# Optimization experiments

Measured on AMD Instinct MI355X. Metric: run time of the kernel, lower is better.

The kernel has to match this reference:

```python
import jax, jax.numpy as jnp
from jax import lax
import numpy as np
import itertools

R = 7            # resolution
N = R * R        # 49 tokens
H = 8            # num_heads
KD = 32          # key_dim
QKD = 2 * H * KD # 512
VD = 2 * KD * H  # 512 (attn_ratio * key_dim * num_heads)
DIM = 384
B = 2048
SCALE = KD ** (-0.5)
BN_EPS = 1e-5


def _bias_idxs():
    points = list(itertools.product(range(R), range(R)))
    offsets = {}
    idxs = []
    for p1 in points:
        for p2 in points:
            o = (abs(p1[0] - p2[0]), abs(p1[1] - p2[1]))
            if o not in offsets:
                offsets[o] = len(offsets)
            idxs.append(offsets[o])
    return np.asarray(idxs, dtype=np.int32).reshape(N, N)  # [49,49], values in [0,49)


def setup_inputs() -> dict:
    key = jax.random.key(0)
    ks = jax.random.split(key, 8)
    return {
        "x": jax.random.normal(ks[0], (B, N, DIM), jnp.float32),
        "pwconv_w": jax.random.normal(ks[1], (QKD + VD, DIM), jnp.float32) * 0.05,
        "pwconv_b": jax.random.normal(ks[2], (QKD + VD,), jnp.float32) * 0.05,
        "dw_w": jax.random.normal(ks[3], (VD, 1, 3, 3), jnp.float32) * 0.1,
        "bn_gamma": jnp.ones((VD,), jnp.float32),
        "bn_beta": jnp.zeros((VD,), jnp.float32),
        "bn_mean": jnp.zeros((VD,), jnp.float32),
        "bn_var": jnp.ones((VD,), jnp.float32),
        "attn_biases": jax.random.normal(ks[4], (H, 49), jnp.float32) * 0.02,
        "proj_w": jax.random.normal(ks[5], (DIM, VD), jnp.float32) * 0.05,
        "proj_b": jnp.zeros((DIM,), jnp.float32),
        "bias_idxs": jnp.asarray(_bias_idxs()),
    }


def reference(x, pwconv_w, pwconv_b, dw_w, bn_gamma, bn_beta, bn_mean, bn_var,
              attn_biases, proj_w, proj_b, bias_idxs):
    b = x.shape[0]
    # [B,N,C] -> [B,C,7,7]
    xc = x.transpose(0, 2, 1).reshape(b, DIM, R, R)
    # 1x1 conv (pointwise) as einsum
    h = jnp.einsum('bchw,oc->bohw', xc, pwconv_w) + pwconv_b[None, :, None, None]
    qk, v1 = h[:, :QKD], h[:, QKD:]
    # [B,512,7,7] -> [B,2,H,KD,N] -> [2,B,H,N,KD]
    qk = qk.reshape(b, 2, H, KD, N).transpose(1, 0, 2, 4, 3)
    q, k = qk[0], qk[1]
    # depthwise 3x3 conv + BN (inference form) + exact GELU, residual into v1
    dw = lax.conv_general_dilated(v1, dw_w, (1, 1), 'SAME',
                                  feature_group_count=VD,
                                  dimension_numbers=('NCHW', 'OIHW', 'NCHW'))
    dw = (dw - bn_mean[None, :, None, None]) * (bn_gamma[None, :, None, None]
          * lax.rsqrt(bn_var[None, :, None, None] + BN_EPS)) + bn_beta[None, :, None, None]
    v1 = v1 + jax.nn.gelu(dw, approximate=False)
    # [B,VD,7,7] -> [B,H,dv,N] -> [B,H,N,dv]
    v = v1.reshape(b, H, VD // H, N).transpose(0, 1, 3, 2)
    bias = attn_biases[:, bias_idxs]  # [H,N,N] gathered relative-position bias
    attn = jax.nn.softmax(jnp.einsum('bhnd,bhmd->bhnm', q, k) * SCALE + bias[None], axis=-1)
    out = jnp.einsum('bhnm,bhmd->bhnd', attn, v).transpose(0, 2, 1, 3).reshape(b, N, VD)
    return out @ proj_w.T + proj_b
```

## Files before the change

### kernel.cpp

```cpp
#include <hip/hip_runtime.h>

#define NPOS 49
#define NH 8
#define DIMC 384
#define VDC 512
#define SCALE_QK 0.17677669529663687f

typedef unsigned short u16;
typedef unsigned int u32;
typedef unsigned char u8;
typedef __attribute__((ext_vector_type(8))) short bf16x8_t;
typedef __attribute__((ext_vector_type(4))) float f32x4_t;

__device__ __forceinline__ u16 f2bf(float f) {
    unsigned u = __float_as_uint(f);
    u = (u + 0x7fffu + ((u >> 16) & 1u)) >> 16;
    return (u16)u;
}
__device__ __forceinline__ float bf2f(u16 b) {
    return __uint_as_float(((unsigned)b) << 16);
}
__device__ __forceinline__ float fastrcp(float x) {
    return __builtin_amdgcn_rcpf(x);
}

__global__ __launch_bounds__(256) void prep_kernel(
    const float* __restrict__ pw, const float* __restrict__ pj,
    u16* __restrict__ wpw, u16* __restrict__ wpj)
{
    int i = blockIdx.x * 256 + threadIdx.x;
    if (i < 1024 * 384) {
        int och = i / 384, k = i - och * 384;
        wpw[((och >> 4) * 12 + (k >> 5)) * 512 + (och & 15) * 32 + (k & 31)] = f2bf(pw[i]);
    }
    if (i < 384 * 512) {
        int o = i / 512, k = i - o * 512;
        wpj[((o >> 4) * 16 + (k >> 5)) * 512 + (o & 15) * 32 + (k & 31)] = f2bf(pj[i]);
    }
}

__global__ __launch_bounds__(512, 2) void fused_kernel(
    const float* __restrict__ x,
    const float* __restrict__ pwb,
    const float* __restrict__ dww,
    const float* __restrict__ bng, const float* __restrict__ bnb,
    const float* __restrict__ bnm, const float* __restrict__ bnv,
    const float* __restrict__ pjb,
    const u16* __restrict__ wpw, const u16* __restrict__ wpj,
    const float* __restrict__ ab, const int* __restrict__ bidx,
    float* __restrict__ out)
{
    __shared__ u16 lds[79056];
    const int tid  = threadIdx.x;
    const int b    = blockIdx.x;
    const int wv   = tid >> 6;
    const int lane = tid & 63;
    const int quad = lane >> 4;
    const int l16  = lane & 15;

    u16* s_q  = lds;
    u16* s_k  = lds + 12544;
    u16* s_v  = lds + 25088;
    u16* s_o2 = lds + 25088;
    u16* s_x  = lds + 57856;
    float* s_abf = (float*)(lds + 77064);
    u8*    s_bidx = (u8*)(lds + 77848);

    {
        const float4* xb4 = (const float4*)(x + (size_t)b * (NPOS * DIMC));
        for (int f = tid; f < NPOS * 96; f += 512) {
            float4 v = xb4[f];
            int row = f / 96;
            int cc  = (f - row * 96) * 4;
            ushort4 w;
            w.x = f2bf(v.x); w.y = f2bf(v.y); w.z = f2bf(v.z); w.w = f2bf(v.w);
            *(ushort4*)(s_x + row * 392 + cc) = w;
        }
        if (tid < 392) s_abf[tid] = ab[tid];
        for (int i = tid; i < 2401; i += 512) s_bidx[i] = (u8)bidx[i];
    }
    __syncthreads();

    int otile[8];
    #pragma unroll
    for (int nt = 0; nt < 8; ++nt)
        otile[nt] = (nt < 2) ? (wv * 2 + nt)
                  : (nt < 4) ? (16 + wv * 2 + (nt - 2))
                  : (32 + wv * 4 + (nt - 4));

    f32x4_t acc[8][4];
    #pragma unroll
    for (int nt = 0; nt < 8; ++nt)
        #pragma unroll
        for (int mt = 0; mt < 4; ++mt)
            acc[nt][mt] = (f32x4_t){0.f, 0.f, 0.f, 0.f};

    #pragma unroll
    for (int ks = 0; ks < 12; ++ks) {
        const int k0 = ks * 32 + quad * 8;
        bf16x8_t afr[4];
        #pragma unroll
        for (int mt = 0; mt < 4; ++mt) {
            int ar = mt * 16 + l16;
            if (ar > 48) ar = 48;
            afr[mt] = *(const bf16x8_t*)(s_x + ar * 392 + k0);
        }
        #pragma unroll
        for (int nt = 0; nt < 8; ++nt) {
            bf16x8_t bfr = *(const bf16x8_t*)(
                wpw + (otile[nt] * 12 + ks) * 512 + l16 * 32 + quad * 8);
            #pragma unroll
            for (int mt = 0; mt < 4; ++mt)
                acc[nt][mt] = __builtin_amdgcn_mfma_f32_16x16x32_bf16(
                    afr[mt], bfr, acc[nt][mt], 0, 0, 0);
        }
    }

    float tap[9];
    #pragma unroll
    for (int j = 0; j < 9; ++j) tap[j] = dww[tid * 9 + j];
    const float bn_scale = bng[tid] * rsqrtf(bnv[tid] + 1e-5f);
    const float bn_shift = bnb[tid] - bnm[tid] * bn_scale;

    #pragma unroll
    for (int nt = 0; nt < 8; ++nt) {
        const int och = otile[nt] * 16 + l16;
        const float bias = pwb[och];
        if (nt < 4) {
            const int d = och & 31;
            u16* base = (nt < 2) ? s_q : s_k;
            #pragma unroll
            for (int mt = 0; mt < 4; ++mt)
                #pragma unroll
                for (int r = 0; r < 4; ++r) {
                    int pos = mt * 16 + quad * 4 + r;
                    if (pos < 49) {
                        int rowi = wv * 49 + pos;
                        int dblk = (d >> 3) ^ ((rowi >> 2) & 3);
                        base[rowi * 32 + (dblk << 3) + (d & 7)] =
                            f2bf(acc[nt][mt][r] + bias);
                    }
                }
        } else {
            const int c  = och - 512;
            const int cb = c & 7;
            u16* vrow = s_v + c * 64;
            #pragma unroll
            for (int mt = 0; mt < 4; ++mt) {
                int pos0 = mt * 16 + quad * 4;
                int jb   = pos0 >> 3;
                int off  = pos0 & 7;
                ushort4 w;
                w.x = f2bf(acc[nt][mt][0] + bias);
                w.y = f2bf(acc[nt][mt][1] + bias);
                w.z = f2bf(acc[nt][mt][2] + bias);
                w.w = f2bf(acc[nt][mt][3] + bias);
                *(ushort4*)(vrow + ((jb ^ cb) << 3) + off) = w;
            }
        }
    }
    asm volatile("s_waitcnt lgkmcnt(0)" ::: "memory");


    {
        const int c  = tid;
        const int cb = c & 7;
        u16* vrow = s_v + c * 64;
        float vv[56];
        #pragma unroll
        for (int jb = 0; jb < 7; ++jb) {
            bf16x8_t t = *(const bf16x8_t*)(vrow + ((jb ^ cb) << 3));
            #pragma unroll
            for (int e = 0; e < 8; ++e) vv[jb * 8 + e] = bf2f((u16)t[e]);
        }
        float res[64];
        #pragma unroll
        for (int y = 0; y < 7; ++y)
            #pragma unroll
            for (int xx = 0; xx < 7; ++xx) {
                float s = 0.f;
                #pragma unroll
                for (int ky = 0; ky < 3; ++ky)
                    #pragma unroll
                    for (int kx = 0; kx < 3; ++kx) {
                        int iy = y + ky - 1, ix = xx + kx - 1;
                        if (iy >= 0 && iy < 7 && ix >= 0 && ix < 7)
                            s += tap[ky * 3 + kx] * vv[iy * 7 + ix];
                    }
                s = s * bn_scale + bn_shift;
                float p2 = s * s;
                float u2 = s * (1.5957691216057308f + 0.0713548162726f * p2);
                float ee = __expf(u2);
                float g  = s * (1.f - fastrcp(ee + 1.f));
                res[y * 7 + xx] = vv[y * 7 + xx] + g;
            }
        #pragma unroll
        for (int i = 49; i < 64; ++i) res[i] = 0.f;
        #pragma unroll
        for (int jb = 0; jb < 8; ++jb) {
            bf16x8_t t;
            #pragma unroll
            for (int e = 0; e < 8; ++e) t[e] = (short)f2bf(res[jb * 8 + e]);
            *(bf16x8_t*)(vrow + ((jb ^ cb) << 3)) = t;
        }
    }
    asm volatile("s_waitcnt lgkmcnt(0)" ::: "memory");

    float invr[4][4];
    {
        const int h = wv;
        bf16x8_t qa[4], kfr[4];
        #pragma unroll
        for (int mt = 0; mt < 4; ++mt) {
            int row = h * 49 + mt * 16 + l16;
            int jq  = quad ^ ((row >> 2) & 3);
            qa[mt] = *(const bf16x8_t*)(s_q + row * 32 + (jq << 3));
        }
        #pragma unroll
        for (int nt = 0; nt < 4; ++nt) {
            int row = h * 49 + nt * 16 + l16;
            int jq  = quad ^ ((row >> 2) & 3);
            kfr[nt] = *(const bf16x8_t*)(s_k + row * 32 + (jq << 3));
        }
        f32x4_t sc[4][4];
        __builtin_amdgcn_s_setprio(1);
        #pragma unroll
        for (int mt = 0; mt < 4; ++mt)
            #pragma unroll
            for (int nt = 0; nt < 4; ++nt) {
                f32x4_t z = (f32x4_t){0.f, 0.f, 0.f, 0.f};
                sc[mt][nt] = __builtin_amdgcn_mfma_f32_16x16x32_bf16(qa[mt], kfr[nt], z, 0, 0, 0);
            }
        __builtin_amdgcn_s_setprio(0);

        float pvreg[4][4][4];
        #pragma unroll
        for (int mt = 0; mt < 4; ++mt)
            #pragma unroll
            for (int r = 0; r < 4; ++r) {
                const int qrow = mt * 16 + quad * 4 + r;
                float e[4];
                #pragma unroll
                for (int nt = 0; nt < 4; ++nt) {
                    const int key = nt * 16 + l16;
                    float val = sc[mt][nt][r] * SCALE_QK;
                    if (key < 49 && qrow < 49)
                        val += s_abf[h * 49 + s_bidx[qrow * 49 + key]];
                    else
                        val = -1e30f;
                    e[nt] = __expf(val);
                }
                float sum = (e[0] + e[1]) + (e[2] + e[3]);
                #pragma unroll
                for (int off = 1; off < 16; off <<= 1)
                    sum += __shfl_xor(sum, off);
                invr[mt][r] = fastrcp(sum);
                pvreg[mt][r][0] = e[0]; pvreg[mt][r][1] = e[1];
                pvreg[mt][r][2] = e[2]; pvreg[mt][r][3] = e[3];
            }

        #pragma unroll
        for (int mt = 0; mt < 4; ++mt)
            #pragma unroll
            for (int r = 0; r < 4; ++r) {
                const int qrow = mt * 16 + quad * 4 + r;
                if (qrow < 49) {
                    const int rowi = h * 49 + qrow;
                    const int sw = (rowi >> 2) & 3;
                    u16* rq = s_q + rowi * 32;
                    u16* rk = s_k + rowi * 32;
                    #pragma unroll
                    for (int nt = 0; nt < 4; ++nt) {
                        const int key = nt * 16 + l16;
                        const int kk  = key & 31;
                        u16* basep = (nt < 2) ? rq : rk;
                        basep[(((kk >> 3) ^ sw) << 3) + (kk & 7)] =
                            f2bf(pvreg[mt][r][nt]);
                    }
                }
            }
        asm volatile("s_waitcnt lgkmcnt(0)" ::: "memory");

        f32x4_t oa[4][4];
        #pragma unroll
        for (int mt = 0; mt < 4; ++mt)
            #pragma unroll
            for (int nt = 0; nt < 4; ++nt)
                oa[mt][nt] = (f32x4_t){0.f, 0.f, 0.f, 0.f};
        #pragma unroll
        for (int ksv = 0; ksv < 2; ++ksv) {
            u16* pbase = ksv ? s_k : s_q;
            bf16x8_t pa[4], vb[4];
            #pragma unroll
            for (int mt = 0; mt < 4; ++mt) {
                int rowi = h * 49 + mt * 16 + l16;
                int jq   = quad ^ ((rowi >> 2) & 3);
                pa[mt] = *(const bf16x8_t*)(pbase + rowi * 32 + (jq << 3));
            }
            #pragma unroll
            for (int nt = 0; nt < 4; ++nt) {
                int rv = h * 64 + nt * 16 + l16;
                vb[nt] = *(const bf16x8_t*)(s_v + rv * 64 + (((ksv * 4 + quad) ^ (rv & 7)) << 3));
            }
            __builtin_amdgcn_s_setprio(1);
            #pragma unroll
            for (int mt = 0; mt < 4; ++mt)
                #pragma unroll
                for (int nt = 0; nt < 4; ++nt)
                    oa[mt][nt] = __builtin_amdgcn_mfma_f32_16x16x32_bf16(
                        pa[mt], vb[nt], oa[mt][nt], 0, 0, 0);
            __builtin_amdgcn_s_setprio(0);
        }
        __syncthreads();
        #pragma unroll
        for (int mt = 0; mt < 4; ++mt)
            #pragma unroll
            for (int nt = 0; nt < 4; ++nt)
                #pragma unroll
                for (int r = 0; r < 4; ++r) {
                    int pos = mt * 16 + quad * 4 + r;
                    if (pos < 49)
                        s_o2[pos * 520 + h * 64 + nt * 16 + l16] =
                            f2bf(oa[mt][nt][r] * invr[mt][r]);
                }
    }
    __syncthreads();

    {
        f32x4_t pacc[3][4];
        #pragma unroll
        for (int ntl = 0; ntl < 3; ++ntl)
            #pragma unroll
            for (int mt = 0; mt < 4; ++mt)
                pacc[ntl][mt] = (f32x4_t){0.f, 0.f, 0.f, 0.f};
        #pragma unroll
        for (int ks = 0; ks < 16; ++ks) {
            const int k0 = ks * 32 + quad * 8;
            bf16x8_t afr[4];
            #pragma unroll
            for (int mt = 0; mt < 4; ++mt)
                afr[mt] = *(const bf16x8_t*)(s_o2 + (mt * 16 + l16) * 520 + k0);
            #pragma unroll
            for (int ntl = 0; ntl < 3; ++ntl) {
                bf16x8_t wb = *(const bf16x8_t*)(
                    wpj + ((wv * 3 + ntl) * 16 + ks) * 512 + l16 * 32 + quad * 8);
                #pragma unroll
                for (int mt = 0; mt < 4; ++mt)
                    pacc[ntl][mt] = __builtin_amdgcn_mfma_f32_16x16x32_bf16(
                        afr[mt], wb, pacc[ntl][mt], 0, 0, 0);
            }
        }
        float* ob = out + (size_t)b * (NPOS * DIMC);
        #pragma unroll
        for (int ntl = 0; ntl < 3; ++ntl) {
            const int o = (wv * 3 + ntl) * 16 + l16;
            const float pb = pjb[o];
            #pragma unroll
            for (int mt = 0; mt < 4; ++mt)
                #pragma unroll
                for (int r = 0; r < 4; ++r) {
                    int pos = mt * 16 + quad * 4 + r;
                    if (pos < 49) ob[pos * 384 + o] = pacc[ntl][mt][r] + pb;
                }
        }
    }
}

extern "C" void kernel_launch(void* const* d_in, const int* in_sizes, int n_in,
                              void* d_out, int out_size, void* d_ws, size_t ws_size,
                              hipStream_t stream)
{
    const float* x   = (const float*)d_in[0];
    const float* pw  = (const float*)d_in[1];
    const float* pwb = (const float*)d_in[2];
    const float* dww = (const float*)d_in[3];
    const float* bng = (const float*)d_in[4];
    const float* bnb = (const float*)d_in[5];
    const float* bnm = (const float*)d_in[6];
    const float* bnv = (const float*)d_in[7];
    const float* ab  = (const float*)d_in[8];
    const float* pj  = (const float*)d_in[9];
    const float* pjb = (const float*)d_in[10];
    const int*  bidx = (const int*)d_in[11];
    float* out = (float*)d_out;

    u16* wpw = (u16*)d_ws;
    u16* wpj = wpw + 1024 * 384;

    const int nb = in_sizes[0] / (NPOS * DIMC);

    prep_kernel<<<1536, 256, 0, stream>>>(pw, pj, wpw, wpj);
    fused_kernel<<<nb, 512, 0, stream>>>(x, pwb, dww, bng, bnb, bnm, bnv, pjb,
                                         wpw, wpj, ab, bidx, out);
}
```

Baseline: 586.6 us.

## Shrink LDS footprint to raise occupancy by streaming x from global and splitting GEMM

Drops the shared-memory staging of x and reads bf16-converted A fragments straight from global memory. The pointwise GEMM is split into a V pass and a later Q/K pass so each wave holds fewer accumulators. Each wave now uses its own small LDS region, and V is redistributed through register shuffles instead of being stored in LDS. Softmax normalisation moves before the PV product, and several LDS layouts gain XOR swizzles. Together these cut LDS from about 158KB to about 61KB, allowing 4 blocks per CU in the launch bounds, at the cost of reading x from global twice and doing more shuffle work.

```diff
diff --git a/kernel.cpp b/kernel.cpp
--- a/kernel.cpp
+++ b/kernel.cpp
@@ -5,12 +5,14 @@
 #define DIMC 384
 #define VDC 512
 #define SCALE_QK 0.17677669529663687f
+#define HS 3584
 
 typedef unsigned short u16;
 typedef unsigned int u32;
 typedef unsigned char u8;
 typedef __attribute__((ext_vector_type(8))) short bf16x8_t;
 typedef __attribute__((ext_vector_type(4))) float f32x4_t;
+typedef __attribute__((ext_vector_type(2))) u32 u32x2_t;
 
 __device__ __forceinline__ u16 f2bf(float f) {
     unsigned u = __float_as_uint(f);
@@ -22,6 +24,21 @@
 }
 __device__ __forceinline__ float fastrcp(float x) {
     return __builtin_amdgcn_rcpf(x);
+}
+__device__ __forceinline__ u32 cvt_pk_bf16(float a, float b) {
+    u32 r;
+    asm("v_cvt_pk_bf16_f32 %0, %1, %2" : "=v"(r) : "v"(a), "v"(b));
+    return r;
+}
+__device__ __forceinline__ bf16x8_t load_x_frag(const float* p) {
+    float4 a = *(const float4*)(p);
+    float4 b = *(const float4*)(p + 4);
+    union { u32 u[4]; bf16x8_t v; } r;
+    r.u[0] = cvt_pk_bf16(a.x, a.y);
+    r.u[1] = cvt_pk_bf16(a.z, a.w);
+    r.u[2] = cvt_pk_bf16(b.x, b.y);
+    r.u[3] = cvt_pk_bf16(b.z, b.w);
+    return r.v;
 }
 
 __global__ __launch_bounds__(256) void prep_kernel(
@@ -39,7 +56,7 @@
     }
 }
 
-__global__ __launch_bounds__(512, 2) void fused_kernel(
+__global__ __launch_bounds__(512, 4) void fused_kernel(
     const float* __restrict__ x,
     const float* __restrict__ pwb,
     const float* __restrict__ dww,
@@ -50,7 +67,7 @@
     const float* __restrict__ ab, const int* __restrict__ bidx,
     float* __restrict__ out)
 {
-    __shared__ u16 lds[79056];
+    __shared__ u16 lds[30660];
     const int tid  = threadIdx.x;
     const int b    = blockIdx.x;
     const int wv   = tid >> 6;
@@ -58,42 +75,25 @@
     const int quad = lane >> 4;
     const int l16  = lane & 15;
 
-    u16* s_q  = lds;
-    u16* s_k  = lds + 12544;
-    u16* s_v  = lds + 25088;
-    u16* s_o2 = lds + 25088;
-    u16* s_x  = lds + 57856;
-    float* s_abf = (float*)(lds + 77064);
-    u8*    s_bidx = (u8*)(lds + 77848);
-
-    {
-        const float4* xb4 = (const float4*)(x + (size_t)b * (NPOS * DIMC));
-        for (int f = tid; f < NPOS * 96; f += 512) {
-            float4 v = xb4[f];
-            int row = f / 96;
-            int cc  = (f - row * 96) * 4;
-            ushort4 w;
-            w.x = f2bf(v.x); w.y = f2bf(v.y); w.z = f2bf(v.z); w.w = f2bf(v.w);
-            *(ushort4*)(s_x + row * 392 + cc) = w;
-        }
-        if (tid < 392) s_abf[tid] = ab[tid];
-        for (int i = tid; i < 2401; i += 512) s_bidx[i] = (u8)bidx[i];
-    }
+    u16* S    = lds + wv * HS;
+    u16* Sq   = S;
+    u16* Sk   = S + 1568;
+    u16* s_o2 = lds;
+    float* s_abf  = (float*)(lds + 28672);
+    u8*    s_bidx = (u8*)(lds + 29456);
+
+    if (tid < 392) s_abf[tid] = ab[tid];
+    for (int i = tid; i < 2401; i += 512) s_bidx[i] = (u8)bidx[i];
     __syncthreads();
 
-    int otile[8];
+    const float* xb = x + (size_t)b * (NPOS * DIMC);
+
+    f32x4_t acc[4][4];
     #pragma unroll
-    for (int nt = 0; nt < 8; ++nt)
-        otile[nt] = (nt < 2) ? (wv * 2 + nt)
-                  : (nt < 4) ? (16 + wv * 2 + (nt - 2))
-                  : (32 + wv * 4 + (nt - 4));
-
-    f32x4_t acc[8][4];
-    #pragma unroll
-    for (int nt = 0; nt < 8; ++nt)
+    for (int t = 0; t < 4; ++t)
         #pragma unroll
         for (int mt = 0; mt < 4; ++mt)
-            acc[nt][mt] = (f32x4_t){0.f, 0.f, 0.f, 0.f};
+            acc[t][mt] = (f32x4_t){0.f, 0.f, 0.f, 0.f};
 
     #pragma unroll
     for (int ks = 0; ks < 12; ++ks) {
@@ -103,77 +103,56 @@
         for (int mt = 0; mt < 4; ++mt) {
             int ar = mt * 16 + l16;
             if (ar > 48) ar = 48;
-            afr[mt] = *(const bf16x8_t*)(s_x + ar * 392 + k0);
-        }
-        #pragma unroll
-        for (int nt = 0; nt < 8; ++nt) {
+            afr[mt] = load_x_frag(xb + ar * 384 + k0);
+        }
+        #pragma unroll
+        for (int vt = 0; vt < 4; ++vt) {
             bf16x8_t bfr = *(const bf16x8_t*)(
-                wpw + (otile[nt] * 12 + ks) * 512 + l16 * 32 + quad * 8);
-            #pragma unroll
-            for (int mt = 0; mt < 4; ++mt)
-                acc[nt][mt] = __builtin_amdgcn_mfma_f32_16x16x32_bf16(
-                    afr[mt], bfr, acc[nt][mt], 0, 0, 0);
-        }
-    }
+                wpw + ((32 + wv * 4 + vt) * 12 + ks) * 512 + l16 * 32 + quad * 8);
+            #pragma unroll
+            for (int mt = 0; mt < 4; ++mt)
+                acc[vt][mt] = __builtin_amdgcn_mfma_f32_16x16x32_bf16(
+                    afr[mt], bfr, acc[vt][mt], 0, 0, 0);
+        }
+    }
+    #pragma unroll
+    for (int vt = 0; vt < 4; ++vt) {
+        const int ch = vt * 16 + l16;
+        const float bias = pwb[512 + wv * 64 + ch];
+        #pragma unroll
+        for (int mt = 0; mt < 4; ++mt) {
+            int pos0 = mt * 16 + quad * 4;
+            if (pos0 < 49) {
+                u32x2_t w;
+                w.x = cvt_pk_bf16(acc[vt][mt][0] + bias, acc[vt][mt][1] + bias);
+                w.y = cvt_pk_bf16(acc[vt][mt][2] + bias, acc[vt][mt][3] + bias);
+                *(u32x2_t*)(S + ch * 56 + pos0) = w;
+            }
+        }
+    }
+    asm volatile("s_waitcnt lgkmcnt(0)" ::: "memory");
 
     float tap[9];
     #pragma unroll
     for (int j = 0; j < 9; ++j) tap[j] = dww[tid * 9 + j];
-    const float bn_scale = bng[tid] * rsqrtf(bnv[tid] + 1e-5f);
-    const float bn_shift = bnb[tid] - bnm[tid] * bn_scale;
-
-    #pragma unroll
-    for (int nt = 0; nt < 8; ++nt) {
-        const int och = otile[nt] * 16 + l16;
-        const float bias = pwb[och];
-        if (nt < 4) {
-            const int d = och & 31;
-            u16* base = (nt < 2) ? s_q : s_k;
-            #pragma unroll
-            for (int mt = 0; mt < 4; ++mt)
-                #pragma unroll
-                for (int r = 0; r < 4; ++r) {
-                    int pos = mt * 16 + quad * 4 + r;
-                    if (pos < 49) {
-                        int rowi = wv * 49 + pos;
-                        int dblk = (d >> 3) ^ ((rowi >> 2) & 3);
-                        base[rowi * 32 + (dblk << 3) + (d & 7)] =
-                            f2bf(acc[nt][mt][r] + bias);
-                    }
-                }
-        } else {
-            const int c  = och - 512;
-            const int cb = c & 7;
-            u16* vrow = s_v + c * 64;
-            #pragma unroll
-            for (int mt = 0; mt < 4; ++mt) {
-                int pos0 = mt * 16 + quad * 4;
-                int jb   = pos0 >> 3;
-                int off  = pos0 & 7;
-                ushort4 w;
-                w.x = f2bf(acc[nt][mt][0] + bias);
-                w.y = f2bf(acc[nt][mt][1] + bias);
-                w.z = f2bf(acc[nt][mt][2] + bias);
-                w.w = f2bf(acc[nt][mt][3] + bias);
-                *(ushort4*)(vrow + ((jb ^ cb) << 3) + off) = w;
-            }
-        }
-    }
-    asm volatile("s_waitcnt lgkmcnt(0)" ::: "memory");
-
-
+    const float bsc = bng[tid] * rsqrtf(bnv[tid] + 1e-5f);
+    const float bsh = bnb[tid] - bnm[tid] * bsc;
+
+    u32 pr[32];
     {
-        const int c  = tid;
-        const int cb = c & 7;
-        u16* vrow = s_v + c * 64;
-        float vv[56];
-        #pragma unroll
-        for (int jb = 0; jb < 7; ++jb) {
-            bf16x8_t t = *(const bf16x8_t*)(vrow + ((jb ^ cb) << 3));
-            #pragma unroll
-            for (int e = 0; e < 8; ++e) vv[jb * 8 + e] = bf2f((u16)t[e]);
-        }
-        float res[64];
+        bf16x8_t tv[7];
+        #pragma unroll
+        for (int jb = 0; jb < 7; ++jb)
+            tv[jb] = *(const bf16x8_t*)(S + lane * 56 + jb * 8);
+        float vv[49];
+        #pragma unroll
+        for (int jb = 0; jb < 7; ++jb)
+            #pragma unroll
+            for (int e = 0; e < 8; ++e) {
+                int p = jb * 8 + e;
+                if (p < 49) vv[p] = bf2f((u16)tv[jb][e]);
+            }
+        float prev = 0.f;
         #pragma unroll
         for (int y = 0; y < 7; ++y)
             #pragma unroll
@@ -187,55 +166,97 @@
                         if (iy >= 0 && iy < 7 && ix >= 0 && ix < 7)
                             s += tap[ky * 3 + kx] * vv[iy * 7 + ix];
                     }
-                s = s * bn_scale + bn_shift;
+                s = s * bsc + bsh;
                 float p2 = s * s;
                 float u2 = s * (1.5957691216057308f + 0.0713548162726f * p2);
                 float ee = __expf(u2);
                 float g  = s * (1.f - fastrcp(ee + 1.f));
-                res[y * 7 + xx] = vv[y * 7 + xx] + g;
-            }
-        #pragma unroll
-        for (int i = 49; i < 64; ++i) res[i] = 0.f;
-        #pragma unroll
-        for (int jb = 0; jb < 8; ++jb) {
-            bf16x8_t t;
-            #pragma unroll
-            for (int e = 0; e < 8; ++e) t[e] = (short)f2bf(res[jb * 8 + e]);
-            *(bf16x8_t*)(vrow + ((jb ^ cb) << 3)) = t;
+                float rs = vv[y * 7 + xx] + g;
+                int p = y * 7 + xx;
+                if ((p & 1) == 0) prev = rs;
+                else              pr[p >> 1] = cvt_pk_bf16(prev, rs);
+            }
+        pr[24] = cvt_pk_bf16(prev, 0.f);
+        #pragma unroll
+        for (int j = 25; j < 32; ++j) pr[j] = 0;
+    }
+
+    {
+        f32x4_t acc2[4][4];
+        #pragma unroll
+        for (int t = 0; t < 4; ++t)
+            #pragma unroll
+            for (int mt = 0; mt < 4; ++mt)
+                acc2[t][mt] = (f32x4_t){0.f, 0.f, 0.f, 0.f};
+        const int tq0 = wv * 2, tq2 = 16 + wv * 2;
+        #pragma unroll
+        for (int ks = 0; ks < 12; ++ks) {
+            const int k0 = ks * 32 + quad * 8;
+            bf16x8_t afr[4];
+            #pragma unroll
+            for (int mt = 0; mt < 4; ++mt) {
+                int ar = mt * 16 + l16;
+                if (ar > 48) ar = 48;
+                afr[mt] = load_x_frag(xb + ar * 384 + k0);
+            }
+            #pragma unroll
+            for (int it = 0; it < 4; ++it) {
+                const int tile = (it < 2) ? (tq0 + it) : (tq2 + it - 2);
+                bf16x8_t bfr = *(const bf16x8_t*)(
+                    wpw + (tile * 12 + ks) * 512 + l16 * 32 + quad * 8);
+                #pragma unroll
+                for (int mt = 0; mt < 4; ++mt)
+                    acc2[it][mt] = __builtin_amdgcn_mfma_f32_16x16x32_bf16(
+                        afr[mt], bfr, acc2[it][mt], 0, 0, 0);
+            }
+        }
+        #pragma unroll
+        for (int it = 0; it < 4; ++it) {
+            const int tile = (it < 2) ? (tq0 + it) : (tq2 + it - 2);
+            const int d = ((it & 1) << 4) + l16;
+            const float bias = pwb[tile * 16 + l16];
+            u16* base = (it < 2) ? Sq : Sk;
+            #pragma unroll
+            for (int mt = 0; mt < 4; ++mt)
+                #pragma unroll
+                for (int r = 0; r < 4; ++r) {
+                    int pos = mt * 16 + quad * 4 + r;
+                    if (pos < 49) {
+                        int dblk = (d >> 3) ^ ((pos >> 2) & 3);
+                        base[pos * 32 + (dblk << 3) + (d & 7)] =
+                            f2bf(acc2[it][mt][r] + bias);
+                    }
+                }
         }
     }
     asm volatile("s_waitcnt lgkmcnt(0)" ::: "memory");
 
-    float invr[4][4];
     {
-        const int h = wv;
         bf16x8_t qa[4], kfr[4];
         #pragma unroll
         for (int mt = 0; mt < 4; ++mt) {
-            int row = h * 49 + mt * 16 + l16;
-            int jq  = quad ^ ((row >> 2) & 3);
-            qa[mt] = *(const bf16x8_t*)(s_q + row * 32 + (jq << 3));
+            int row = mt * 16 + l16;
+            if (row > 48) row = 48;
+            int jq = quad ^ ((row >> 2) & 3);
+            qa[mt] = *(const bf16x8_t*)(Sq + row * 32 + (jq << 3));
         }
         #pragma unroll
         for (int nt = 0; nt < 4; ++nt) {
-            int row = h * 49 + nt * 16 + l16;
-            int jq  = quad ^ ((row >> 2) & 3);
-            kfr[nt] = *(const bf16x8_t*)(s_k + row * 32 + (jq << 3));
-        }
-        f32x4_t sc[4][4];
-        __builtin_amdgcn_s_setprio(1);
-        #pragma unroll
-        for (int mt = 0; mt < 4; ++mt)
+            int row = nt * 16 + l16;
+            if (row > 48) row = 48;
+            int jq = quad ^ ((row >> 2) & 3);
+            kfr[nt] = *(const bf16x8_t*)(Sk + row * 32 + (jq << 3));
+        }
+        #pragma unroll
+        for (int mt = 0; mt < 4; ++mt) {
+            f32x4_t sc[4];
+            __builtin_amdgcn_s_setprio(1);
             #pragma unroll
             for (int nt = 0; nt < 4; ++nt) {
                 f32x4_t z = (f32x4_t){0.f, 0.f, 0.f, 0.f};
-                sc[mt][nt] = __builtin_amdgcn_mfma_f32_16x16x32_bf16(qa[mt], kfr[nt], z, 0, 0, 0);
-            }
-        __builtin_amdgcn_s_setprio(0);
-
-        float pvreg[4][4][4];
-        #pragma unroll
-        for (int mt = 0; mt < 4; ++mt)
+                sc[nt] = __builtin_amdgcn_mfma_f32_16x16x32_bf16(qa[mt], kfr[nt], z, 0, 0, 0);
+            }
+            __builtin_amdgcn_s_setprio(0);
             #pragma unroll
             for (int r = 0; r < 4; ++r) {
                 const int qrow = mt * 16 + quad * 4 + r;
@@ -243,9 +264,9 @@
                 #pragma unroll
                 for (int nt = 0; nt < 4; ++nt) {
                     const int key = nt * 16 + l16;
-                    float val = sc[mt][nt][r] * SCALE_QK;
+                    float val = sc[nt][r] * SCALE_QK;
                     if (key < 49 && qrow < 49)
-                        val += s_abf[h * 49 + s_bidx[qrow * 49 + key]];
+                        val += s_abf[wv * 49 + s_bidx[qrow * 49 + key]];
                     else
                         val = -1e30f;
                     e[nt] = __expf(val);
@@ -254,32 +275,38 @@
                 #pragma unroll
                 for (int off = 1; off < 16; off <<= 1)
                     sum += __shfl_xor(sum, off);
-                invr[mt][r] = fastrcp(sum);
-                pvreg[mt][r][0] = e[0]; pvreg[mt][r][1] = e[1];
-                pvreg[mt][r][2] = e[2]; pvreg[mt][r][3] = e[3];
-            }
-
-        #pragma unroll
-        for (int mt = 0; mt < 4; ++mt)
-            #pragma unroll
-            for (int r = 0; r < 4; ++r) {
-                const int qrow = mt * 16 + quad * 4 + r;
+                const float inv = fastrcp(sum);
                 if (qrow < 49) {
-                    const int rowi = h * 49 + qrow;
-                    const int sw = (rowi >> 2) & 3;
-                    u16* rq = s_q + rowi * 32;
-                    u16* rk = s_k + rowi * 32;
+                    const int sw = qrow & 7;
                     #pragma unroll
                     for (int nt = 0; nt < 4; ++nt) {
                         const int key = nt * 16 + l16;
-                        const int kk  = key & 31;
-                        u16* basep = (nt < 2) ? rq : rk;
-                        basep[(((kk >> 3) ^ sw) << 3) + (kk & 7)] =
-                            f2bf(pvreg[mt][r][nt]);
+                        S[qrow * 64 + (((key >> 3) ^ sw) << 3) + (key & 7)] =
+                            f2bf(e[nt] * inv);
                     }
                 }
             }
+        }
         asm volatile("s_waitcnt lgkmcnt(0)" ::: "memory");
+
+        bf16x8_t vbf[2][4];
+        #pragma unroll
+        for (int ksv = 0; ksv < 2; ++ksv)
+            #pragma unroll
+            for (int nt = 0; nt < 4; ++nt) {
+                union { u32 u[4]; bf16x8_t v; } cc;
+                const int src = nt * 16 + l16;
+                #pragma unroll
+                for (int w = 0; w < 4; ++w) {
+                    u32 t0 = __shfl(pr[ksv * 16 + 0 + w],  src);
+                    u32 t1 = __shfl(pr[ksv * 16 + 4 + w],  src);
+                    u32 t2 = __shfl(pr[ksv * 16 + 8 + w],  src);
+                    u32 t3 = __shfl(pr[ksv * 16 + 12 + w], src);
+                    cc.u[w] = (quad & 2) ? ((quad & 1) ? t3 : t2)
+                                         : ((quad & 1) ? t1 : t0);
+                }
+                vbf[ksv][nt] = cc.v;
+            }
 
         f32x4_t oa[4][4];
         #pragma unroll
@@ -289,18 +316,13 @@
                 oa[mt][nt] = (f32x4_t){0.f, 0.f, 0.f, 0.f};
         #pragma unroll
         for (int ksv = 0; ksv < 2; ++ksv) {
-            u16* pbase = ksv ? s_k : s_q;
-            bf16x8_t pa[4], vb[4];
+            bf16x8_t pa[4];
             #pragma unroll
             for (int mt = 0; mt < 4; ++mt) {
-                int rowi = h * 49 + mt * 16 + l16;
-                int jq   = quad ^ ((rowi >> 2) & 3);
-                pa[mt] = *(const bf16x8_t*)(pbase + rowi * 32 + (jq << 3));
-            }
-            #pragma unroll
-            for (int nt = 0; nt < 4; ++nt) {
-                int rv = h * 64 + nt * 16 + l16;
-                vb[nt] = *(const bf16x8_t*)(s_v + rv * 64 + (((ksv * 4 + quad) ^ (rv & 7)) << 3));
+                int rp = mt * 16 + l16;
+                if (rp > 48) rp = 48;
+                int slot = (ksv * 4 + quad) ^ (rp & 7);
+                pa[mt] = *(const bf16x8_t*)(S + rp * 64 + (slot << 3));
             }
             __builtin_amdgcn_s_setprio(1);
             #pragma unroll
@@ -308,10 +330,11 @@
                 #pragma unroll
                 for (int nt = 0; nt < 4; ++nt)
                     oa[mt][nt] = __builtin_amdgcn_mfma_f32_16x16x32_bf16(
-                        pa[mt], vb[nt], oa[mt][nt], 0, 0, 0);
+                        pa[mt], vbf[ksv][nt], oa[mt][nt], 0, 0, 0);
             __builtin_amdgcn_s_setprio(0);
         }
         __syncthreads();
+
         #pragma unroll
         for (int mt = 0; mt < 4; ++mt)
             #pragma unroll
@@ -319,9 +342,12 @@
                 #pragma unroll
                 for (int r = 0; r < 4; ++r) {
                     int pos = mt * 16 + quad * 4 + r;
-                    if (pos < 49)
-                        s_o2[pos * 520 + h * 64 + nt * 16 + l16] =
-                            f2bf(oa[mt][nt][r] * invr[mt][r]);
+                    if (pos < 49) {
+                        int col = wv * 64 + nt * 16 + l16;
+                        int slot = (col >> 3) ^ (pos & 7);
+                        s_o2[pos * 512 + (slot << 3) + (col & 7)] =
+                            f2bf(oa[mt][nt][r]);
+                    }
                 }
     }
     __syncthreads();
@@ -335,11 +361,14 @@
                 pacc[ntl][mt] = (f32x4_t){0.f, 0.f, 0.f, 0.f};
         #pragma unroll
         for (int ks = 0; ks < 16; ++ks) {
-            const int k0 = ks * 32 + quad * 8;
             bf16x8_t afr[4];
             #pragma unroll
-            for (int mt = 0; mt < 4; ++mt)
-                afr[mt] = *(const bf16x8_t*)(s_o2 + (mt * 16 + l16) * 520 + k0);
+            for (int mt = 0; mt < 4; ++mt) {
+                int row = mt * 16 + l16;
+                if (row > 48) row = 48;
+                int slot = (ks * 4 + quad) ^ (row & 7);
+                afr[mt] = *(const bf16x8_t*)(s_o2 + row * 512 + (slot << 3));
+            }
             #pragma unroll
             for (int ntl = 0; ntl < 3; ++ntl) {
                 bf16x8_t wb = *(const bf16x8_t*)(
```

Result: slower. 794.5 us (+35.4%).

## Split pointwise GEMM into two staggered phases and use packed bf16 conversion

Applied to the files above, without the earlier changes.

Each wave now computes its pointwise-conv output in two phases of four tiles instead of all eight tiles at once. This halves the live MFMA accumulators and lowers register pressure. Waves 0-3 do their V tiles plus the depthwise-conv/GELU first, while waves 4-7 start with Q/K, so MFMA work and VALU-heavy work from different waves can overlap. Software round-to-nearest-even bf16 conversion is replaced by the hardware v_cvt_pk_bf16_f32 instruction with packed stores. The trade-off is that the x tile in LDS is re-read for the A fragments in each phase, and the staggered schedule depends on the wave-to-channel mapping staying wave-local.

```diff
diff --git a/kernel.cpp b/kernel.cpp
--- a/kernel.cpp
+++ b/kernel.cpp
@@ -11,11 +11,15 @@
 typedef unsigned char u8;
 typedef __attribute__((ext_vector_type(8))) short bf16x8_t;
 typedef __attribute__((ext_vector_type(4))) float f32x4_t;
-
+typedef __attribute__((ext_vector_type(2))) u32 u32x2_t;
+
+__device__ __forceinline__ u32 cvt_pk_bf16(float a, float b) {
+    u32 r;
+    asm("v_cvt_pk_bf16_f32 %0, %1, %2" : "=v"(r) : "v"(a), "v"(b));
+    return r;
+}
 __device__ __forceinline__ u16 f2bf(float f) {
-    unsigned u = __float_as_uint(f);
-    u = (u + 0x7fffu + ((u >> 16) & 1u)) >> 16;
-    return (u16)u;
+    return (u16)cvt_pk_bf16(f, f);
 }
 __device__ __forceinline__ float bf2f(u16 b) {
     return __uint_as_float(((unsigned)b) << 16);
@@ -63,7 +67,7 @@
     u16* s_v  = lds + 25088;
     u16* s_o2 = lds + 25088;
     u16* s_x  = lds + 57856;
-    float* s_abf = (float*)(lds + 77064);
+    float* s_abf  = (float*)(lds + 77064);
     u8*    s_bidx = (u8*)(lds + 77848);
 
     {
@@ -72,139 +76,151 @@
             float4 v = xb4[f];
             int row = f / 96;
             int cc  = (f - row * 96) * 4;
-            ushort4 w;
-            w.x = f2bf(v.x); w.y = f2bf(v.y); w.z = f2bf(v.z); w.w = f2bf(v.w);
-            *(ushort4*)(s_x + row * 392 + cc) = w;
+            u32x2_t w;
+            w.x = cvt_pk_bf16(v.x, v.y);
+            w.y = cvt_pk_bf16(v.z, v.w);
+            *(u32x2_t*)(s_x + row * 392 + cc) = w;
         }
         if (tid < 392) s_abf[tid] = ab[tid];
         for (int i = tid; i < 2401; i += 512) s_bidx[i] = (u8)bidx[i];
     }
     __syncthreads();
-
-    int otile[8];
-    #pragma unroll
-    for (int nt = 0; nt < 8; ++nt)
-        otile[nt] = (nt < 2) ? (wv * 2 + nt)
-                  : (nt < 4) ? (16 + wv * 2 + (nt - 2))
-                  : (32 + wv * 4 + (nt - 4));
-
-    f32x4_t acc[8][4];
-    #pragma unroll
-    for (int nt = 0; nt < 8; ++nt)
-        #pragma unroll
-        for (int mt = 0; mt < 4; ++mt)
-            acc[nt][mt] = (f32x4_t){0.f, 0.f, 0.f, 0.f};
-
-    #pragma unroll
-    for (int ks = 0; ks < 12; ++ks) {
-        const int k0 = ks * 32 + quad * 8;
-        bf16x8_t afr[4];
-        #pragma unroll
-        for (int mt = 0; mt < 4; ++mt) {
-            int ar = mt * 16 + l16;
-            if (ar > 48) ar = 48;
-            afr[mt] = *(const bf16x8_t*)(s_x + ar * 392 + k0);
-        }
-        #pragma unroll
-        for (int nt = 0; nt < 8; ++nt) {
-            bf16x8_t bfr = *(const bf16x8_t*)(
-                wpw + (otile[nt] * 12 + ks) * 512 + l16 * 32 + quad * 8);
-            #pragma unroll
-            for (int mt = 0; mt < 4; ++mt)
-                acc[nt][mt] = __builtin_amdgcn_mfma_f32_16x16x32_bf16(
-                    afr[mt], bfr, acc[nt][mt], 0, 0, 0);
-        }
-    }
 
     float tap[9];
     #pragma unroll
     for (int j = 0; j < 9; ++j) tap[j] = dww[tid * 9 + j];
-    const float bn_scale = bng[tid] * rsqrtf(bnv[tid] + 1e-5f);
-    const float bn_shift = bnb[tid] - bnm[tid] * bn_scale;
-
-    #pragma unroll
-    for (int nt = 0; nt < 8; ++nt) {
-        const int och = otile[nt] * 16 + l16;
-        const float bias = pwb[och];
-        if (nt < 4) {
-            const int d = och & 31;
-            u16* base = (nt < 2) ? s_q : s_k;
+    const float bsc = bng[tid] * rsqrtf(bnv[tid] + 1e-5f);
+    const float bsh = bnb[tid] - bnm[tid] * bsc;
+
+    #pragma unroll 1
+    for (int phase = 0; phase < 2; ++phase) {
+        const int doV = (phase == 0) ^ (wv >= 4 ? 1 : 0);
+
+        int tl[4];
+        if (doV) {
+            tl[0] = 32 + wv * 4; tl[1] = tl[0] + 1; tl[2] = tl[0] + 2; tl[3] = tl[0] + 3;
+        } else {
+            tl[0] = wv * 2; tl[1] = wv * 2 + 1; tl[2] = 16 + wv * 2; tl[3] = 17 + wv * 2;
+        }
+
+        f32x4_t acc[4][4];
+        #pragma unroll
+        for (int t = 0; t < 4; ++t)
             #pragma unroll
             for (int mt = 0; mt < 4; ++mt)
-                #pragma unroll
-                for (int r = 0; r < 4; ++r) {
-                    int pos = mt * 16 + quad * 4 + r;
-                    if (pos < 49) {
-                        int rowi = wv * 49 + pos;
-                        int dblk = (d >> 3) ^ ((rowi >> 2) & 3);
-                        base[rowi * 32 + (dblk << 3) + (d & 7)] =
-                            f2bf(acc[nt][mt][r] + bias);
+                acc[t][mt] = (f32x4_t){0.f, 0.f, 0.f, 0.f};
+
+        #pragma unroll
+        for (int ks = 0; ks < 12; ++ks) {
+            const int k0 = ks * 32 + quad * 8;
+            bf16x8_t afr[4];
+            #pragma unroll
+            for (int mt = 0; mt < 4; ++mt) {
+                int ar = mt * 16 + l16;
+                if (ar > 48) ar = 48;
+                afr[mt] = *(const bf16x8_t*)(s_x + ar * 392 + k0);
+            }
+            #pragma unroll
+            for (int t = 0; t < 4; ++t) {
+                bf16x8_t bfr = *(const bf16x8_t*)(
+                    wpw + (tl[t] * 12 + ks) * 512 + l16 * 32 + quad * 8);
+                #pragma unroll
+                for (int mt = 0; mt < 4; ++mt)
+                    acc[t][mt] = __builtin_amdgcn_mfma_f32_16x16x32_bf16(
+                        afr[mt], bfr, acc[t][mt], 0, 0, 0);
+            }
+        }
+
+        if (doV) {
+            #pragma unroll
+            for (int vt = 0; vt < 4; ++vt) {
+                const int c  = wv * 64 + vt * 16 + l16;
+                const int cb = c & 7;
+                const float bias = pwb[512 + c];
+                u16* vrow = s_v + c * 64;
+                #pragma unroll
+                for (int mt = 0; mt < 4; ++mt) {
+                    int pos0 = mt * 16 + quad * 4;
+                    if (pos0 < 49) {
+                        int jb  = pos0 >> 3;
+                        int off = pos0 & 7;
+                        u32x2_t w;
+                        w.x = cvt_pk_bf16(acc[vt][mt][0] + bias, acc[vt][mt][1] + bias);
+                        w.y = cvt_pk_bf16(acc[vt][mt][2] + bias, acc[vt][mt][3] + bias);
+                        *(u32x2_t*)(vrow + ((jb ^ cb) << 3) + off) = w;
                     }
                 }
+            }
+            asm volatile("s_waitcnt lgkmcnt(0)" ::: "memory");
+
+            {
+                const int c  = tid;
+                const int cb = c & 7;
+                u16* vrow = s_v + c * 64;
+                float vv[56];
+                #pragma unroll
+                for (int jb = 0; jb < 7; ++jb) {
+                    bf16x8_t t = *(const bf16x8_t*)(vrow + ((jb ^ cb) << 3));
+                    #pragma unroll
+                    for (int e = 0; e < 8; ++e) vv[jb * 8 + e] = bf2f((u16)t[e]);
+                }
+                float res[64];
+                #pragma unroll
+                for (int y = 0; y < 7; ++y)
+                    #pragma unroll
+                    for (int xx = 0; xx < 7; ++xx) {
+                        float s = 0.f;
+                        #pragma unroll
+                        for (int ky = 0; ky < 3; ++ky)
+                            #pragma unroll
+                            for (int kx = 0; kx < 3; ++kx) {
+                                int iy = y + ky - 1, ix = xx + kx - 1;
+                                if (iy >= 0 && iy < 7 && ix >= 0 && ix < 7)
+                                    s += tap[ky * 3 + kx] * vv[iy * 7 + ix];
+                            }
+                        s = s * bsc + bsh;
+                        float p2 = s * s;
+                        float u2 = s * (1.5957691216057308f + 0.0713548162726f * p2);
+                        float ee = __expf(u2);
+                        float g  = s * (1.f - fastrcp(ee + 1.f));
+                        res[y * 7 + xx] = vv[y * 7 + xx] + g;
+                    }
+                #pragma unroll
+                for (int i = 49; i < 64; ++i) res[i] = 0.f;
+                #pragma unroll
+                for (int jb = 0; jb < 8; ++jb) {
+                    u32x2_t w0, w1;
+                    w0.x = cvt_pk_bf16(res[jb * 8 + 0], res[jb * 8 + 1]);
+                    w0.y = cvt_pk_bf16(res[jb * 8 + 2], res[jb * 8 + 3]);
+                    w1.x = cvt_pk_bf16(res[jb * 8 + 4], res[jb * 8 + 5]);
+                    w1.y = cvt_pk_bf16(res[jb * 8 + 6], res[jb * 8 + 7]);
+                    *(u32x2_t*)(vrow + ((jb ^ cb) << 3))     = w0;
+                    *(u32x2_t*)(vrow + ((jb ^ cb) << 3) + 4) = w1;
+                }
+            }
+            asm volatile("s_waitcnt lgkmcnt(0)" ::: "memory");
         } else {
-            const int c  = och - 512;
-            const int cb = c & 7;
-            u16* vrow = s_v + c * 64;
-            #pragma unroll
-            for (int mt = 0; mt < 4; ++mt) {
-                int pos0 = mt * 16 + quad * 4;
-                int jb   = pos0 >> 3;
-                int off  = pos0 & 7;
-                ushort4 w;
-                w.x = f2bf(acc[nt][mt][0] + bias);
-                w.y = f2bf(acc[nt][mt][1] + bias);
-                w.z = f2bf(acc[nt][mt][2] + bias);
-                w.w = f2bf(acc[nt][mt][3] + bias);
-                *(ushort4*)(vrow + ((jb ^ cb) << 3) + off) = w;
-            }
-        }
-    }
-    asm volatile("s_waitcnt lgkmcnt(0)" ::: "memory");
-
-
-    {
-        const int c  = tid;
-        const int cb = c & 7;
-        u16* vrow = s_v + c * 64;
-        float vv[56];
-        #pragma unroll
-        for (int jb = 0; jb < 7; ++jb) {
-            bf16x8_t t = *(const bf16x8_t*)(vrow + ((jb ^ cb) << 3));
-            #pragma unroll
-            for (int e = 0; e < 8; ++e) vv[jb * 8 + e] = bf2f((u16)t[e]);
-        }
-        float res[64];
-        #pragma unroll
-        for (int y = 0; y < 7; ++y)
-            #pragma unroll
-            for (int xx = 0; xx < 7; ++xx) {
-                float s = 0.f;
-                #pragma unroll
-                for (int ky = 0; ky < 3; ++ky)
+            #pragma unroll
+            for (int it = 0; it < 4; ++it) {
+                const int d = ((it & 1) << 4) + l16;
+                const float bias = pwb[tl[it] * 16 + l16];
+                u16* base = (it < 2) ? s_q : s_k;
+                #pragma unroll
+                for (int mt = 0; mt < 4; ++mt)
                     #pragma unroll
-                    for (int kx = 0; kx < 3; ++kx) {
-                        int iy = y + ky - 1, ix = xx + kx - 1;
-                        if (iy >= 0 && iy < 7 && ix >= 0 && ix < 7)
-                            s += tap[ky * 3 + kx] * vv[iy * 7 + ix];
+                    for (int r = 0; r < 4; ++r) {
+                        int pos = mt * 16 + quad * 4 + r;
+                        if (pos < 49) {
+                            int rowi = wv * 49 + pos;
+                            int dblk = (d >> 3) ^ ((rowi >> 2) & 3);
+                            base[rowi * 32 + (dblk << 3) + (d & 7)] =
+                                f2bf(acc[it][mt][r] + bias);
+                        }
                     }
-                s = s * bn_scale + bn_shift;
-                float p2 = s * s;
-                float u2 = s * (1.5957691216057308f + 0.0713548162726f * p2);
-                float ee = __expf(u2);
-                float g  = s * (1.f - fastrcp(ee + 1.f));
-                res[y * 7 + xx] = vv[y * 7 + xx] + g;
-            }
-        #pragma unroll
-        for (int i = 49; i < 64; ++i) res[i] = 0.f;
-        #pragma unroll
-        for (int jb = 0; jb < 8; ++jb) {
-            bf16x8_t t;
-            #pragma unroll
-            for (int e = 0; e < 8; ++e) t[e] = (short)f2bf(res[jb * 8 + e]);
-            *(bf16x8_t*)(vrow + ((jb ^ cb) << 3)) = t;
-        }
-    }
-    asm volatile("s_waitcnt lgkmcnt(0)" ::: "memory");
+            }
+            asm volatile("s_waitcnt lgkmcnt(0)" ::: "memory");
+        }
+    }
 
     float invr[4][4];
     {
```

Result: slower. 645.6 us (+10.1%).
